# Kernel tuning notes

Hardware: AMD Instinct MI355X
Metric: run time of the kernel (lower is better)

The kernel has to match this reference:

```python
import jax, jax.numpy as jnp
import numpy as np

N_ATOMS = 50000
NUM_ELEM = 10
LMAX = 3            # 4 instructions -> l = 0..3
C_IN = 128
C_OUT = 128
SH_DIM = (LMAX + 1) ** 2  # 16


def setup_inputs() -> dict:
    key = jax.random.key(0)
    kx, ks, kw = jax.random.split(key, 3)
    x = jax.random.normal(kx, (N_ATOMS, SH_DIM, C_IN), dtype=jnp.float32)
    species = jax.random.randint(ks, (N_ATOMS,), 0, NUM_ELEM)
    y = jax.nn.one_hot(species, NUM_ELEM, dtype=jnp.float32)  # one-hot element encoding
    weights = jax.random.normal(kw, (NUM_ELEM, LMAX + 1, C_IN, C_OUT), dtype=jnp.float32)
    return {"x": x, "y": y, "weights": weights}


def reference(x, y, weights):
    # x: [N, 16, C_in]; y: [N, E] one-hot; weights: [E, 4, C_in, C_out]
    # For each l, rows l^2 .. (l+1)^2 of the SH axis get a per-element linear map.
    # path_weight (e3nn Linear normalization) = 1/sqrt(fan_in).
    scale = jnp.asarray(1.0 / np.sqrt(C_IN), dtype=x.dtype)
    E = weights.shape[0]
    outs = []
    for l in range(LMAX + 1):
        s, e = l * l, (l + 1) * (l + 1)
        xl = x[:, s:e, :]                         # [N, 2l+1, C_in]
        acc = jnp.zeros((x.shape[0], e - s, weights.shape[-1]), dtype=x.dtype)
        # small fixed loop over element species; avoids materializing per-atom
        # [N, C_in, C_out] gathered weights
        for el in range(E):
            acc = acc + y[:, el, None, None] * (xl @ weights[el, l])
        outs.append(acc * scale)
    return jnp.concatenate(outs, axis=1)          # [N, 16, C_out]
```

## Files before the change

### kernel.cpp

```cpp
#include <hip/hip_runtime.h>
#include <hip/hip_bf16.h>
#include <stdint.h>


#define NATOMS 50000
#define NELEM  10
#define SHD    16
#define CC     128
#define APB    16
#define TPS    ((NATOMS + APB - 1) / APB)
#define KP     40

typedef __attribute__((ext_vector_type(8))) short bf16x8;
typedef __attribute__((ext_vector_type(4))) float f32x4;

__device__ __forceinline__ unsigned short f2bf(float f) {
    union { float f; uint32_t u; } v; v.f = f;
    return (unsigned short)((v.u + 0x7FFFu + ((v.u >> 16) & 1u)) >> 16);
}

__device__ __forceinline__ int l_of_m(int m) {
    return (m == 0) ? 0 : (m < 4) ? 1 : (m < 9) ? 2 : 3;
}

__global__ void k_count(const float* __restrict__ y,
                        int* __restrict__ counts, int* __restrict__ species) {
    int n = blockIdx.x * 256 + threadIdx.x;
    if (n >= NATOMS) return;
    int s = 0;
    #pragma unroll
    for (int j = 0; j < NELEM; ++j)
        if (y[(size_t)n * NELEM + j] > 0.5f) s = j;
    species[n] = s;
    atomicAdd(&counts[s], 1);
}

__global__ void k_offsets(const int* __restrict__ counts, int* __restrict__ offsets) {
    if (blockIdx.x == 0 && threadIdx.x == 0) {
        int acc = 0;
        for (int e2 = 0; e2 < NELEM; ++e2) { offsets[e2] = acc; acc += counts[e2]; }
    }
}

__global__ void k_scatter(const int* __restrict__ species, const int* __restrict__ offsets,
                          int* __restrict__ cursors, int* __restrict__ idxb) {
    int n = blockIdx.x * 256 + threadIdx.x;
    if (n >= NATOMS) return;
    int s = species[n];
    int p = atomicAdd(&cursors[s], 1);
    idxb[offsets[s] + p] = n;
}

__global__ void k_twt(const float* __restrict__ w, unsigned short* __restrict__ wt) {
    int i = blockIdx.x * 256 + threadIdx.x;
    if (i >= NELEM * 4 * CC * CC) return;
    int c  = i & 127;
    int k  = (i >> 7) & 127;
    int el = i >> 14;
    wt[((size_t)el * CC + c) * CC + k] = f2bf(w[i]);
}

__global__ __launch_bounds__(256, 2)
void k_main(const float* __restrict__ x,
            const unsigned short* __restrict__ wt,
            const int* __restrict__ counts,
            const int* __restrict__ offsets,
            const int* __restrict__ idxb,
            float* __restrict__ out) {
    int e = blockIdx.x % NELEM;
    int t = blockIdx.x / NELEM;
    int cnt = counts[e];
    int a0 = t * APB;
    if (a0 >= cnt) return;
    int nrem = cnt - a0; if (nrem > APB) nrem = APB;
    int base = offsets[e] + a0;

    __shared__ unsigned short wsl[4 * CC * KP];

    int tid  = threadIdx.x;
    int lane = tid & 63;
    int wv   = tid >> 6;
    int quad = lane >> 4;
    int l16  = lane & 15;

    int aid = idxb[base + ((l16 < nrem) ? l16 : 0)];
    const float* xa = x + (size_t)aid * (SHD * CC);
    const unsigned short* wte = wt + (size_t)e * (4 * CC * CC);

    f32x4 acc[4][8];
    #pragma unroll
    for (int i = 0; i < 4; ++i)
        #pragma unroll
        for (int j = 0; j < 8; ++j)
            acc[i][j] = (f32x4){0.f, 0.f, 0.f, 0.f};

    for (int kt = 0; kt < 4; ++kt) {
        #pragma unroll
        for (int i = 0; i < 8; ++i) {
            int ch  = i * 256 + tid;
            int row = ch >> 2;
            int j16 = ch & 3;
            uint4 v = *(const uint4*)(wte + (size_t)row * CC + kt * 32 + j16 * 8);
            *(uint4*)(&wsl[row * KP + j16 * 8]) = v;
        }
        __syncthreads();

        bf16x8 bfr[8];
        int lprev = -1;
        #pragma unroll
        for (int mi = 0; mi < 4; ++mi) {
            int m = wv * 4 + mi;
            int l = l_of_m(m);
            const float* xp = xa + m * CC + kt * 32 + quad * 8;
            float4 x0 = *(const float4*)(xp);
            float4 x1 = *(const float4*)(xp + 4);
            bf16x8 afr;
            afr[0] = (short)f2bf(x0.x); afr[1] = (short)f2bf(x0.y);
            afr[2] = (short)f2bf(x0.z); afr[3] = (short)f2bf(x0.w);
            afr[4] = (short)f2bf(x1.x); afr[5] = (short)f2bf(x1.y);
            afr[6] = (short)f2bf(x1.z); afr[7] = (short)f2bf(x1.w);
            if (l != lprev) {
                #pragma unroll
                for (int n = 0; n < 8; ++n) {
                    int col = n * 16 + l16;
                    bfr[n] = *(const bf16x8*)(&wsl[(l * CC + col) * KP + quad * 8]);
                }
                lprev = l;
            }
            #pragma unroll
            for (int n = 0; n < 8; ++n)
                acc[mi][n] = __builtin_amdgcn_mfma_f32_16x16x32_bf16(afr, bfr[n], acc[mi][n], 0, 0, 0);
        }
        __syncthreads();
    }

    const float scale = 0.08838834764831845f;
    int aidr[4];
    #pragma unroll
    for (int r = 0; r < 4; ++r) {
        int a = quad * 4 + r;
        aidr[r] = idxb[base + ((a < nrem) ? a : 0)];
    }
    #pragma unroll
    for (int mi = 0; mi < 4; ++mi) {
        int m = wv * 4 + mi;
        #pragma unroll
        for (int n = 0; n < 8; ++n) {
            #pragma unroll
            for (int r = 0; r < 4; ++r) {
                int a = quad * 4 + r;
                if (a < nrem) {
                    out[(size_t)aidr[r] * (SHD * CC) + m * CC + n * 16 + l16] =
                        acc[mi][n][r] * scale;
                }
            }
        }
    }
}

extern "C" void kernel_launch(void* const* d_in, const int* in_sizes, int n_in,
                              void* d_out, int out_size, void* d_ws, size_t ws_size,
                              hipStream_t stream) {
    const float* x = (const float*)d_in[0];
    const float* y = (const float*)d_in[1];
    const float* w = (const float*)d_in[2];
    float* out = (float*)d_out;

    char* ws = (char*)d_ws;
    int* counts  = (int*)(ws);
    int* cursors = (int*)(ws + 64);
    int* offsets = (int*)(ws + 128);
    int* species = (int*)(ws + 192);
    int* idxb    = (int*)(ws + 192 + NATOMS * 4);
    unsigned short* wt = (unsigned short*)(ws + 192 + 2 * NATOMS * 4 + 64);

    hipMemsetAsync(d_ws, 0, 192, stream);
    k_count  <<<(NATOMS + 255) / 256, 256, 0, stream>>>(y, counts, species);
    k_twt    <<<(NELEM * 4 * CC * CC + 255) / 256, 256, 0, stream>>>(w, wt);
    k_offsets<<<1, 64, 0, stream>>>(counts, offsets);
    k_scatter<<<(NATOMS + 255) / 256, 256, 0, stream>>>(species, offsets, cursors, idxb);
    k_main   <<<NELEM * TPS, 256, 0, stream>>>(x, wt, counts, offsets, idxb, out);
}
```

Baseline: 1.046 ms.

## Tile sorted atoms contiguously, read weights directly, aggregate histogram atomics per wave

The main kernel now takes 16 consecutive entries of the species-sorted index list per block and drops the per-species tile grid, which removes the many blocks that exited early. Each block loops over the distinct species in its tile and reads bf16 weights straight from global/L2 instead of staging them through LDS with barriers. It also preloads and converts all of x into registers once. The 1/sqrt(C_in) scale is folded into the weight conversion. Counting and scatter now use wave ballots with a single atomic per species per wave, and species is packed into the index word. Tiles that span two species do redundant MFMA work, and the weight fragments lose LDS reuse, which relies on L2 bandwidth. NTILES = NATOMS/APB assumes an exact multiple, which holds for 50000/16.

```diff
diff --git a/kernel.cpp b/kernel.cpp
--- a/kernel.cpp
+++ b/kernel.cpp
@@ -8,8 +8,7 @@
 #define SHD    16
 #define CC     128
 #define APB    16
-#define TPS    ((NATOMS + APB - 1) / APB)
-#define KP     40
+#define NTILES (NATOMS / APB)
 
 typedef __attribute__((ext_vector_type(8))) short bf16x8;
 typedef __attribute__((ext_vector_type(4))) float f32x4;
@@ -25,14 +24,22 @@
 
 __global__ void k_count(const float* __restrict__ y,
                         int* __restrict__ counts, int* __restrict__ species) {
-    int n = blockIdx.x * 256 + threadIdx.x;
-    if (n >= NATOMS) return;
-    int s = 0;
+    int n    = blockIdx.x * 256 + threadIdx.x;
+    int lane = threadIdx.x & 63;
+    int s = -1;
+    if (n < NATOMS) {
+        s = 0;
+        #pragma unroll
+        for (int j = 0; j < NELEM; ++j)
+            if (y[(size_t)n * NELEM + j] > 0.5f) s = j;
+        species[n] = s;
+    }
     #pragma unroll
-    for (int j = 0; j < NELEM; ++j)
-        if (y[(size_t)n * NELEM + j] > 0.5f) s = j;
-    species[n] = s;
-    atomicAdd(&counts[s], 1);
+    for (int e = 0; e < NELEM; ++e) {
+        unsigned long long m = __ballot(s == e);
+        if (m != 0ull && lane == (__ffsll(m) - 1))
+            atomicAdd(&counts[e], __popcll(m));
+    }
 }
 
 __global__ void k_offsets(const int* __restrict__ counts, int* __restrict__ offsets) {
@@ -44,11 +51,22 @@
 
 __global__ void k_scatter(const int* __restrict__ species, const int* __restrict__ offsets,
                           int* __restrict__ cursors, int* __restrict__ idxb) {
-    int n = blockIdx.x * 256 + threadIdx.x;
-    if (n >= NATOMS) return;
-    int s = species[n];
-    int p = atomicAdd(&cursors[s], 1);
-    idxb[offsets[s] + p] = n;
+    int n    = blockIdx.x * 256 + threadIdx.x;
+    int lane = threadIdx.x & 63;
+    int s = (n < NATOMS) ? species[n] : -1;
+    #pragma unroll
+    for (int e = 0; e < NELEM; ++e) {
+        unsigned long long m = __ballot(s == e);
+        if (m == 0ull) continue;
+        int leader = __ffsll(m) - 1;
+        int bp = 0;
+        if (lane == leader) bp = atomicAdd(&cursors[e], __popcll(m));
+        bp = __shfl(bp, leader, 64);
+        if (s == e) {
+            int pos = __popcll(m & ((1ull << lane) - 1ull));
+            idxb[offsets[e] + bp + pos] = (n << 4) | s;
+        }
+    }
 }
 
 __global__ void k_twt(const float* __restrict__ w, unsigned short* __restrict__ wt) {
@@ -57,101 +75,103 @@
     int c  = i & 127;
     int k  = (i >> 7) & 127;
     int el = i >> 14;
-    wt[((size_t)el * CC + c) * CC + k] = f2bf(w[i]);
+    wt[((size_t)el * CC + c) * CC + k] = f2bf(w[i] * 0.08838834764831845f);
 }
 
 __global__ __launch_bounds__(256, 2)
 void k_main(const float* __restrict__ x,
             const unsigned short* __restrict__ wt,
-            const int* __restrict__ counts,
-            const int* __restrict__ offsets,
             const int* __restrict__ idxb,
             float* __restrict__ out) {
-    int e = blockIdx.x % NELEM;
-    int t = blockIdx.x / NELEM;
-    int cnt = counts[e];
-    int a0 = t * APB;
-    if (a0 >= cnt) return;
-    int nrem = cnt - a0; if (nrem > APB) nrem = APB;
-    int base = offsets[e] + a0;
-
-    __shared__ unsigned short wsl[4 * CC * KP];
-
+    int t    = blockIdx.x;
+    int base = t * APB;
     int tid  = threadIdx.x;
     int lane = tid & 63;
     int wv   = tid >> 6;
     int quad = lane >> 4;
     int l16  = lane & 15;
 
-    int aid = idxb[base + ((l16 < nrem) ? l16 : 0)];
+    int pk   = idxb[base + l16];
+    int aid  = pk >> 4;
+    int mysp = pk & 15;
     const float* xa = x + (size_t)aid * (SHD * CC);
-    const unsigned short* wte = wt + (size_t)e * (4 * CC * CC);
-
-    f32x4 acc[4][8];
-    #pragma unroll
-    for (int i = 0; i < 4; ++i)
-        #pragma unroll
-        for (int j = 0; j < 8; ++j)
-            acc[i][j] = (f32x4){0.f, 0.f, 0.f, 0.f};
-
-    for (int kt = 0; kt < 4; ++kt) {
-        #pragma unroll
-        for (int i = 0; i < 8; ++i) {
-            int ch  = i * 256 + tid;
-            int row = ch >> 2;
-            int j16 = ch & 3;
-            uint4 v = *(const uint4*)(wte + (size_t)row * CC + kt * 32 + j16 * 8);
-            *(uint4*)(&wsl[row * KP + j16 * 8]) = v;
-        }
-        __syncthreads();
-
-        bf16x8 bfr[8];
-        int lprev = -1;
-        #pragma unroll
-        for (int mi = 0; mi < 4; ++mi) {
-            int m = wv * 4 + mi;
-            int l = l_of_m(m);
-            const float* xp = xa + m * CC + kt * 32 + quad * 8;
-            float4 x0 = *(const float4*)(xp);
-            float4 x1 = *(const float4*)(xp + 4);
-            bf16x8 afr;
-            afr[0] = (short)f2bf(x0.x); afr[1] = (short)f2bf(x0.y);
-            afr[2] = (short)f2bf(x0.z); afr[3] = (short)f2bf(x0.w);
-            afr[4] = (short)f2bf(x1.x); afr[5] = (short)f2bf(x1.y);
-            afr[6] = (short)f2bf(x1.z); afr[7] = (short)f2bf(x1.w);
-            if (l != lprev) {
-                #pragma unroll
-                for (int n = 0; n < 8; ++n) {
-                    int col = n * 16 + l16;
-                    bfr[n] = *(const bf16x8*)(&wsl[(l * CC + col) * KP + quad * 8]);
-                }
-                lprev = l;
-            }
-            #pragma unroll
-            for (int n = 0; n < 8; ++n)
-                acc[mi][n] = __builtin_amdgcn_mfma_f32_16x16x32_bf16(afr, bfr[n], acc[mi][n], 0, 0, 0);
-        }
-        __syncthreads();
-    }
-
-    const float scale = 0.08838834764831845f;
-    int aidr[4];
-    #pragma unroll
-    for (int r = 0; r < 4; ++r) {
-        int a = quad * 4 + r;
-        aidr[r] = idxb[base + ((a < nrem) ? a : 0)];
-    }
+
+    bf16x8 axr[4][4];
     #pragma unroll
     for (int mi = 0; mi < 4; ++mi) {
-        int m = wv * 4 + mi;
-        #pragma unroll
-        for (int n = 0; n < 8; ++n) {
+        const float* xp = xa + (wv * 4 + mi) * CC + quad * 8;
+        float4 v0[4], v1[4];
+        #pragma unroll
+        for (int kt = 0; kt < 4; ++kt) {
+            v0[kt] = *(const float4*)(xp + kt * 32);
+            v1[kt] = *(const float4*)(xp + kt * 32 + 4);
+        }
+        #pragma unroll
+        for (int kt = 0; kt < 4; ++kt) {
+            bf16x8 a;
+            a[0] = (short)f2bf(v0[kt].x); a[1] = (short)f2bf(v0[kt].y);
+            a[2] = (short)f2bf(v0[kt].z); a[3] = (short)f2bf(v0[kt].w);
+            a[4] = (short)f2bf(v1[kt].x); a[5] = (short)f2bf(v1[kt].y);
+            a[6] = (short)f2bf(v1[kt].z); a[7] = (short)f2bf(v1[kt].w);
+            axr[mi][kt] = a;
+        }
+    }
+
+    unsigned rem = 0xFFFFu;
+    while (rem) {
+        int r0 = __ffs((int)rem) - 1;
+        int e  = __shfl(mysp, r0, 64);
+        unsigned long long bal = __ballot(mysp == e);
+        unsigned mask16 = (unsigned)(bal & 0xFFFFull);
+        rem &= ~mask16;
+
+        const unsigned short* wte = wt + (size_t)e * (4 * CC * CC);
+
+        f32x4 acc[4][8];
+        #pragma unroll
+        for (int i = 0; i < 4; ++i)
             #pragma unroll
-            for (int r = 0; r < 4; ++r) {
-                int a = quad * 4 + r;
-                if (a < nrem) {
-                    out[(size_t)aidr[r] * (SHD * CC) + m * CC + n * 16 + l16] =
-                        acc[mi][n][r] * scale;
+            for (int j = 0; j < 8; ++j)
+                acc[i][j] = (f32x4){0.f, 0.f, 0.f, 0.f};
+
+        #pragma unroll
+        for (int kt = 0; kt < 4; ++kt) {
+            bf16x8 bfr[8];
+            int lprev = -1;
+            #pragma unroll
+            for (int mi = 0; mi < 4; ++mi) {
+                int l = l_of_m(wv * 4 + mi);
+                if (l != lprev) {
+                    #pragma unroll
+                    for (int n = 0; n < 8; ++n)
+                        bfr[n] = *(const bf16x8*)(wte
+                            + ((size_t)(l * CC + n * 16 + l16)) * CC
+                            + kt * 32 + quad * 8);
+                    lprev = l;
+                }
+                #pragma unroll
+                for (int n = 0; n < 8; ++n)
+                    acc[mi][n] = __builtin_amdgcn_mfma_f32_16x16x32_bf16(
+                        axr[mi][kt], bfr[n], acc[mi][n], 0, 0, 0);
+            }
+        }
+
+        int  aidr[4]; bool st[4];
+        #pragma unroll
+        for (int r = 0; r < 4; ++r) {
+            int row = quad * 4 + r;
+            aidr[r] = __shfl(aid, row, 64);
+            st[r]   = (mask16 >> row) & 1u;
+        }
+        #pragma unroll
+        for (int mi = 0; mi < 4; ++mi) {
+            #pragma unroll
+            for (int n = 0; n < 8; ++n) {
+                #pragma unroll
+                for (int r = 0; r < 4; ++r) {
+                    if (st[r])
+                        out[(size_t)aidr[r] * (SHD * CC) + (wv * 4 + mi) * CC
+                            + n * 16 + l16] = acc[mi][n][r];
                 }
             }
         }
@@ -179,5 +199,5 @@
     k_twt    <<<(NELEM * 4 * CC * CC + 255) / 256, 256, 0, stream>>>(w, wt);
     k_offsets<<<1, 64, 0, stream>>>(counts, offsets);
     k_scatter<<<(NATOMS + 255) / 256, 256, 0, stream>>>(species, offsets, cursors, idxb);
-    k_main   <<<NELEM * TPS, 256, 0, stream>>>(x, wt, counts, offsets, idxb, out);
-}
+    k_main   <<<NTILES, 256, 0, stream>>>(x, wt, idxb, out);
+}
```

After: 980.2 us. 6.3% less time.
